# Performance work log

Measured on AMD Instinct MI355X. Metric: run time of the kernel, lower is better.

Reference implementation:

```python
import jax, jax.numpy as jnp
import numpy as np


def _l2norm(x, eps=1e-6):
    # Matches F.normalize(p=2, dim=-1, eps=eps): divide by max(||x||, eps)
    n = jnp.sqrt(jnp.sum(x * x, axis=-1, keepdims=True))
    return x / jnp.maximum(n, eps)


def setup_inputs() -> dict:
    key = jax.random.key(0)
    k0, k1, k2, k3, k4 = jax.random.split(key, 5)
    B, T, H, Dk, Dv = 2, 4096, 16, 128, 128
    q = _l2norm(jax.random.normal(k0, (B, T, H, Dk), dtype=jnp.float32))
    k = _l2norm(jax.random.normal(k1, (B, T, H, Dk), dtype=jnp.float32))
    v = jax.random.normal(k2, (B, T, H, Dv), dtype=jnp.float32)
    # alpha: decay in (0,1) (module: exp(-exp(A_log)*softplus(a+dt_bias)))
    alpha = jax.random.uniform(k3, (B, T, H), dtype=jnp.float32, minval=0.5, maxval=0.999)
    # beta: write gate in (0,1) (module: sigmoid(b))
    beta = jax.random.uniform(k4, (B, T, H), dtype=jnp.float32, minval=0.01, maxval=0.99)
    initial_state = jnp.zeros((B, H, Dk, Dv), dtype=jnp.float32)
    return {"q": q, "k": k, "v": v, "alpha": alpha, "beta": beta,
            "initial_state": initial_state}


def reference(q, k, v, alpha, beta, initial_state):
    """Gated delta rule recurrence (faithful to gdn_recurrent_naive).

    S_t = a_t * (S_{t-1} - b_t * k_t (k_t^T S_{t-1})) + b_t * k_t v_t^T
    o_t = S_t^T q_t
    """
    def step(S, xs):
        q_t, k_t, v_t, a_t, b_t = xs  # (B,H,Dk), (B,H,Dk), (B,H,Dv), (B,H), (B,H)
        a = a_t[..., None, None]
        b = b_t[..., None, None]
        kS = jnp.einsum('bhd,bhdv->bhv', k_t, S)          # k^T S
        S = a * (S - b * jnp.einsum('bhd,bhv->bhdv', k_t, kS)) \
            + b * jnp.einsum('bhd,bhv->bhdv', k_t, v_t)   # delta-rule update
        o = jnp.einsum('bhdv,bhd->bhv', S, q_t)           # read with q
        return S, o

    xs = (q.swapaxes(0, 1), k.swapaxes(0, 1), v.swapaxes(0, 1),
          alpha.swapaxes(0, 1), beta.swapaxes(0, 1))  # time-major for scan
    S_final, outs = jax.lax.scan(step, initial_state.astype(jnp.float32), xs)
    return outs.swapaxes(0, 1), S_final  # (B,T,H,Dv), (B,H,Dk,Dv)
```

## Files before the change

### kernel.cpp

```cpp
#include <hip/hip_runtime.h>

#define T_LEN 4096
#define H_N   16
#define DK    128
#define DV    128
#define LCH   64
#define NCH   64

typedef float f32x4 __attribute__((ext_vector_type(4)));
typedef short s16x8 __attribute__((ext_vector_type(8)));

#define OFF_U0 0
#define OFF_W  32768
#define OFF_Q  49152
#define OFF_KD 65536
#define OFF_G  81920
#define OFF_GM 90112
#define CH_B   90368ull
#define WS_NEED (2048ull * CH_B)

#define SWZ(row) (((row)&7) << 4)

#define AST 68
#define RST 132

__device__ __forceinline__ unsigned short f2b(float x) {
  unsigned u = __float_as_uint(x);
  return (unsigned short)((u + 0x7FFF + ((u >> 16) & 1)) >> 16);
}

#define GLDS16(gp, lp)                                                        \
  __builtin_amdgcn_global_load_lds(                                           \
      (const __attribute__((address_space(1))) void*)(gp),                    \
      (__attribute__((address_space(3))) void*)(lp), 16, 0, 0)
#define GLDS4(gp, lp)                                                         \
  __builtin_amdgcn_global_load_lds(                                           \
      (const __attribute__((address_space(1))) void*)(gp),                    \
      (__attribute__((address_space(3))) void*)(lp), 4, 0, 0)

#define LBAR()                                                                \
  do {                                                                        \
    asm volatile("s_waitcnt lgkmcnt(0)" ::: "memory");                        \
    __builtin_amdgcn_s_barrier();                                             \
    __builtin_amdgcn_sched_barrier(0);                                        \
  } while (0)

__device__ void solve64(float* RHS, const float* A, int tid) {
#pragma unroll 1
  for (int I = 0; I < 4; ++I) {
    if (I > 0) {
      const int i2 = 16 * I + (tid >> 4), cg = tid & 15;
      float* rp = RHS + i2 * RST + cg * 8;
      f32x4 a0 = *(const f32x4*)(rp);
      f32x4 a1 = *(const f32x4*)(rp + 4);
      for (int j = 0; j < 16 * I; ++j) {
        float a = A[i2 * AST + j];
        const float* yp = RHS + j * RST + cg * 8;
        f32x4 y0 = *(const f32x4*)(yp);
        f32x4 y1 = *(const f32x4*)(yp + 4);
#pragma unroll
        for (int e = 0; e < 4; ++e) {
          a0[e] = fmaf(-a, y0[e], a0[e]);
          a1[e] = fmaf(-a, y1[e], a1[e]);
        }
      }
      *(f32x4*)(rp) = a0;
      *(f32x4*)(rp + 4) = a1;
      __syncthreads();
    }
    if (tid < 128) {
      const int col = tid;
      float y[16];
#pragma unroll
      for (int r = 0; r < 16; ++r) y[r] = RHS[(16 * I + r) * RST + col];
#pragma unroll
      for (int r = 1; r < 16; ++r) {
        float t0 = 0.f, t1 = 0.f;
#pragma unroll
        for (int j = 0; j < 15; ++j)
          if (j < r) {
            float av = A[(16 * I + r) * AST + 16 * I + j];
            if (j & 1) t1 = fmaf(av, y[j], t1);
            else       t0 = fmaf(av, y[j], t0);
          }
        y[r] -= t0 + t1;
      }
#pragma unroll
      for (int r = 0; r < 16; ++r) RHS[(16 * I + r) * RST + col] = y[r];
    }
    __syncthreads();
  }
}

extern "C" __global__ void __launch_bounds__(256) gdn_p1(
    const float* __restrict__ q, const float* __restrict__ k,
    const float* __restrict__ v, const float* __restrict__ al,
    const float* __restrict__ be, char* __restrict__ ws) {
  __shared__ __align__(16) unsigned char big[34048];
  __shared__ __align__(16) float A_s[64 * AST];
  __shared__ float g_s[64], bb_s[64], sc_s[64];
  unsigned char* Kb = big;
  unsigned char* Qb = big + 16384;
  float* RHS = (float*)big;

  const int bid = blockIdx.x;
  const int bh = bid & 31, c = bid >> 5;
  const int b = bh >> 4, h = bh & 15;
  const int tid = threadIdx.x;
  const int t0 = c * LCH;
  char* wsc = ws + (size_t)(bh * 64 + c) * CH_B;

  if (tid < 64) {
    size_t gi = (size_t)(b * T_LEN + t0 + tid) * H_N + h;
    float x = __logf(al[gi]);
    bb_s[tid] = be[gi];
#pragma unroll
    for (int d = 1; d < 64; d <<= 1) {
      float yv = __shfl_up(x, d, 64);
      if (tid >= d) x += yv;
    }
    float gam = __expf(x);
    g_s[tid] = x;
    sc_s[tid] = gam;
    *(float*)(wsc + OFF_GM + tid * 4) = gam;
  }

  for (int idx = tid; idx < 1024; idx += 256) {
    int row = idx >> 4, grp = idx & 15;
    size_t go = ((size_t)(b * T_LEN + t0 + row) * H_N + h) * DK + grp * 8;
    float4 ka = *(const float4*)(k + go);
    float4 kb2 = *(const float4*)(k + go + 4);
    float4 qa = *(const float4*)(q + go);
    float4 qb2 = *(const float4*)(q + go + 4);
    union { unsigned short u[8]; uint4 v4; } tk, tq;
    tk.u[0] = f2b(ka.x); tk.u[1] = f2b(ka.y); tk.u[2] = f2b(ka.z); tk.u[3] = f2b(ka.w);
    tk.u[4] = f2b(kb2.x); tk.u[5] = f2b(kb2.y); tk.u[6] = f2b(kb2.z); tk.u[7] = f2b(kb2.w);
    tq.u[0] = f2b(qa.x); tq.u[1] = f2b(qa.y); tq.u[2] = f2b(qa.z); tq.u[3] = f2b(qa.w);
    tq.u[4] = f2b(qb2.x); tq.u[5] = f2b(qb2.y); tq.u[6] = f2b(qb2.z); tq.u[7] = f2b(qb2.w);
    int la = (row * 256 + grp * 16) ^ SWZ(row);
    *(uint4*)(Kb + la) = tk.v4;
    *(uint4*)(Qb + la) = tq.v4;
    *(uint4*)(wsc + OFF_Q + la) = tq.v4;
  }
  __syncthreads();

  const int w = tid >> 6, l = tid & 63, li = l & 15, hi = l >> 4;
  f32x4 aK[4], aQ[4];
#pragma unroll
  for (int jt = 0; jt < 4; ++jt) { aK[jt] = (f32x4){0, 0, 0, 0}; aQ[jt] = (f32x4){0, 0, 0, 0}; }
#pragma unroll
  for (int ks = 0; ks < 4; ++ks) {
    int rowA = 16 * w + li;
    int oa = (rowA * 256 + ks * 64 + hi * 16) ^ SWZ(rowA);
    s16x8 fa = *(const s16x8*)(Kb + oa);
    s16x8 fq = *(const s16x8*)(Qb + oa);
#pragma unroll
    for (int jt = 0; jt < 4; ++jt) {
      int rowB = 16 * jt + li;
      s16x8 fb = *(const s16x8*)(Kb + ((rowB * 256 + ks * 64 + hi * 16) ^ SWZ(rowB)));
      aK[jt] = __builtin_amdgcn_mfma_f32_16x16x32_bf16(fa, fb, aK[jt], 0, 0, 0);
      aQ[jt] = __builtin_amdgcn_mfma_f32_16x16x32_bf16(fq, fb, aQ[jt], 0, 0, 0);
    }
  }
#pragma unroll
  for (int jt = 0; jt < 4; ++jt)
#pragma unroll
    for (int r = 0; r < 4; ++r) {
      int i = 16 * w + hi * 4 + r, j = 16 * jt + li;
      float e = __expf(g_s[i] - g_s[j]);
      A_s[i * AST + j] = (j < i) ? bb_s[i] * e * aK[jt][r] : 0.f;
      *(unsigned short*)(wsc + OFF_G + ((i * 128 + j * 2) ^ SWZ(i))) =
          f2b((j <= i) ? e * aQ[jt][r] : 0.f);
    }
  __syncthreads();

  for (int idx = tid; idx < 2048; idx += 256) {
    int row = idx >> 5, c4 = idx & 31;
    float4 vv = *(const float4*)(v + ((size_t)(b * T_LEN + t0 + row) * H_N + h) * DV + c4 * 4);
    float s = bb_s[row];
    float4 o = {s * vv.x, s * vv.y, s * vv.z, s * vv.w};
    *(float4*)(RHS + row * RST + c4 * 4) = o;
  }
  __syncthreads();
  solve64(RHS, A_s, tid);
  for (int idx = tid; idx < 2048; idx += 256) {
    int row = idx >> 5, c4 = idx & 31;
    *(float4*)(wsc + OFF_U0 + (c4 >> 2) * 4096 + row * 64 + (c4 & 3) * 16) =
        *(const float4*)(RHS + row * RST + c4 * 4);
  }
  __syncthreads();

  for (int idx = tid; idx < 2048; idx += 256) {
    int row = idx >> 5, c4 = idx & 31;
    float4 kv = *(const float4*)(k + ((size_t)(b * T_LEN + t0 + row) * H_N + h) * DK + c4 * 4);
    float s = bb_s[row] * sc_s[row];
    float4 o = {s * kv.x, s * kv.y, s * kv.z, s * kv.w};
    *(float4*)(RHS + row * RST + c4 * 4) = o;
  }
  __syncthreads();
  solve64(RHS, A_s, tid);
  for (int idx = tid; idx < 1024; idx += 256) {
    int row = idx >> 4, g8 = idx & 15;
    const float* p = RHS + row * RST + g8 * 8;
    union { unsigned short u[8]; uint4 v4; } t;
#pragma unroll
    for (int e = 0; e < 8; ++e) t.u[e] = f2b(-p[e]);
    *(uint4*)(wsc + OFF_W + ((row * 256 + g8 * 16) ^ SWZ(row))) = t.v4;
  }
  __syncthreads();

  if (tid < 64) sc_s[tid] = __expf(g_s[63] - g_s[tid]);
  __syncthreads();
  float* Kf = (float*)big;
#pragma unroll 1
  for (int p = 0; p < 2; ++p) {
    for (int idx = tid; idx < 1024; idx += 256) {
      int r = idx >> 5, c4 = idx & 31;
      float4 kv = *(const float4*)(k + ((size_t)(b * T_LEN + t0 + 32 * p + r) * H_N + h) * DK + c4 * 4);
      *(float4*)(Kf + r * 132 + c4 * 4) = kv;
    }
    __syncthreads();
#pragma unroll
    for (int m = 0; m < 16; ++m) {
      int flat = m * 256 + tid;
      int j32 = flat & 31, d = flat >> 5;
      float val = sc_s[32 * p + j32] * Kf[j32 * 132 + d];
      *(unsigned short*)(wsc + OFF_KD + ((d * 128 + (32 * p + j32) * 2) ^ SWZ(d))) = f2b(val);
    }
    __syncthreads();
  }
}

extern "C" __global__ void __launch_bounds__(512, 1) gdn_p2(
    const float* __restrict__ S0, float* __restrict__ out,
    const char* __restrict__ ws) {
  __shared__ unsigned char Wb[2][16384];
  __shared__ unsigned char Qb[2][16384];
  __shared__ unsigned char KDb[2][16384];
  __shared__ unsigned char Gb[2][8192];
  __shared__ float U0s[2][1024];
  __shared__ float gam[2][64];
  __shared__ unsigned char Stb[4096];
  __shared__ unsigned char Ytb[2048];
  __shared__ float Oa[1024];

  const int bid = blockIdx.x;
  const int bh = bid & 31, s = bid >> 5;
  const int b = bh >> 4, h = bh & 15;
  const int tid = threadIdx.x;
  const int w = tid >> 6;
  const int lane = tid & 63, li = lane & 15, hi = lane >> 4;
  const int wq = w & 3;
  const bool grpA = (w < 4);
  const char* wsbase = ws + (size_t)bh * 64 * CH_B;

#define STG(CI, P)                                                            \
  do {                                                                        \
    const char* c_ = wsbase + (size_t)(CI) * CH_B;                            \
    _Pragma("unroll") for (int j_ = 0; j_ < 2; ++j_) {                        \
      GLDS16(c_ + OFF_W + j_ * 8192 + tid * 16, &Wb[P][j_ * 8192 + w * 1024]); \
      GLDS16(c_ + OFF_Q + j_ * 8192 + tid * 16, &Qb[P][j_ * 8192 + w * 1024]); \
      GLDS16(c_ + OFF_KD + j_ * 8192 + tid * 16, &KDb[P][j_ * 8192 + w * 1024]); \
    }                                                                         \
    GLDS16(c_ + OFF_G + tid * 16, &Gb[P][w * 1024]);                          \
    if (w < 4) GLDS16(c_ + OFF_U0 + s * 4096 + tid * 16,                      \
                      (unsigned char*)U0s[P] + w * 1024);                     \
    if (w == 7) GLDS4(c_ + OFF_GM + lane * 4, &gam[P][0]);                    \
  } while (0)

  float S[2][4];
  if (!grpA) {
#pragma unroll
    for (int t = 0; t < 2; ++t)
#pragma unroll
      for (int r = 0; r < 4; ++r) {
        int d = (wq + 4 * t) * 16 + hi * 4 + r;
        S[t][r] = S0[((size_t)bh * 128 + d) * 128 + s * 16 + li];
      }
  }
#define WRITE_ST()                                                            \
  do {                                                                        \
    _Pragma("unroll") for (int t = 0; t < 2; ++t)                             \
        _Pragma("unroll") for (int r = 0; r < 4; r += 2) {                    \
      int d = (wq + 4 * t) * 16 + hi * 4 + r;                                 \
      unsigned pk = (unsigned)f2b(S[t][r]) | ((unsigned)f2b(S[t][r + 1]) << 16); \
      *(unsigned*)(Stb + ((li * 256 + d * 2) ^ SWZ(li))) = pk;                \
    }                                                                         \
  } while (0)

  STG(0, 0);
  if (!grpA) WRITE_ST();
  __syncthreads();

#pragma unroll 1
  for (int c = 0; c < NCH; ++c) {
    const int p = c & 1;
    if (c + 1 < NCH) STG(c + 1, p ^ 1);

    s16x8 sfb[4];
#pragma unroll
    for (int ks = 0; ks < 4; ++ks)
      sfb[ks] = *(const s16x8*)(Stb + ((li * 256 + ks * 64 + hi * 16) ^ SWZ(li)));

    if (grpA) {
      f32x4 Y;
#pragma unroll
      for (int r = 0; r < 4; ++r) Y[r] = U0s[p][(16 * wq + hi * 4 + r) * 16 + li];
#pragma unroll
      for (int ks = 0; ks < 4; ++ks) {
        s16x8 fa = *(const s16x8*)(Wb[p] + (((16 * wq + li) * 256 + ks * 64 + hi * 16) ^ SWZ(li)));
        Y = __builtin_amdgcn_mfma_f32_16x16x32_bf16(fa, sfb[ks], Y, 0, 0, 0);
      }
#pragma unroll
      for (int r = 0; r < 4; r += 2) {
        int j = 16 * wq + hi * 4 + r;
        unsigned pk = (unsigned)f2b(Y[r]) | ((unsigned)f2b(Y[r + 1]) << 16);
        *(unsigned*)(Ytb + ((li * 128 + j * 2) ^ SWZ(li))) = pk;
      }
      LBAR();
      f32x4 O;
      s16x8 yfb[2];
#pragma unroll
      for (int ks = 0; ks < 2; ++ks)
        yfb[ks] = *(const s16x8*)(Ytb + ((li * 128 + ks * 64 + hi * 16) ^ SWZ(li)));
#pragma unroll
      for (int r = 0; r < 4; ++r) O[r] = Oa[(16 * wq + hi * 4 + r) * 16 + li];
#pragma unroll
      for (int ks = 0; ks < 2; ++ks) {
        s16x8 fa = *(const s16x8*)(Gb[p] + (((16 * wq + li) * 128 + ks * 64 + hi * 16) ^ SWZ(li)));
        O = __builtin_amdgcn_mfma_f32_16x16x32_bf16(fa, yfb[ks], O, 0, 0, 0);
      }
#pragma unroll
      for (int r = 0; r < 4; ++r) {
        size_t oi = ((size_t)(b * T_LEN + c * 64 + 16 * wq + hi * 4 + r) * H_N + h) * DV + s * 16 + li;
        out[oi] = O[r];
      }
    } else {
      f32x4 Oq = {0, 0, 0, 0};
#pragma unroll
      for (int ks = 0; ks < 4; ++ks) {
        s16x8 fa = *(const s16x8*)(Qb[p] + (((16 * wq + li) * 256 + ks * 64 + hi * 16) ^ SWZ(li)));
        Oq = __builtin_amdgcn_mfma_f32_16x16x32_bf16(fa, sfb[ks], Oq, 0, 0, 0);
      }
#pragma unroll
      for (int r = 0; r < 4; ++r) {
        int row = 16 * wq + hi * 4 + r;
        Oa[row * 16 + li] = gam[p][row] * Oq[r];
      }
      LBAR();
      s16x8 yfb[2];
#pragma unroll
      for (int ks = 0; ks < 2; ++ks)
        yfb[ks] = *(const s16x8*)(Ytb + ((li * 128 + ks * 64 + hi * 16) ^ SWZ(li)));
      float ge = gam[p][63];
#pragma unroll
      for (int t = 0; t < 2; ++t) {
        f32x4 acc;
#pragma unroll
        for (int r = 0; r < 4; ++r) acc[r] = ge * S[t][r];
#pragma unroll
        for (int ks = 0; ks < 2; ++ks) {
          s16x8 fa = *(const s16x8*)(KDb[p] + ((((wq + 4 * t) * 16 + li) * 128 + ks * 64 + hi * 16) ^ SWZ(li)));
          acc = __builtin_amdgcn_mfma_f32_16x16x32_bf16(fa, yfb[ks], acc, 0, 0, 0);
        }
#pragma unroll
        for (int r = 0; r < 4; ++r) S[t][r] = acc[r];
      }
      WRITE_ST();
    }
    __syncthreads();
  }

  if (!grpA) {
#pragma unroll
    for (int t = 0; t < 2; ++t)
#pragma unroll
      for (int r = 0; r < 4; ++r) {
        int d = (wq + 4 * t) * 16 + hi * 4 + r;
        out[(size_t)(2 * T_LEN * H_N * DV) + ((size_t)bh * 128 + d) * 128 + s * 16 + li] = S[t][r];
      }
  }
}

#define COLS 16
#define CHUNK 16
#define STEP_B 8192u
#define AB_B 64u
#define OSTRIDE (H_N * DV)
template <int CTRL>
__device__ __forceinline__ float dpp_add(float x) {
  int y = __builtin_amdgcn_update_dpp(0, __float_as_int(x), CTRL, 0xF, 0xF, true);
  return x + __int_as_float(y);
}
__device__ __forceinline__ float red16(float x) {
  x = dpp_add<0xB1>(x); x = dpp_add<0x4E>(x);
  x = dpp_add<0x124>(x); x = dpp_add<0x128>(x);
  return x;
}
extern "C" __global__ void __launch_bounds__(256, 1) gdn_fallback(
    const float* __restrict__ q, const float* __restrict__ k,
    const float* __restrict__ v, const float* __restrict__ al,
    const float* __restrict__ be, const float* __restrict__ S0,
    float* __restrict__ out) {
  __shared__ float kb[2][CHUNK * DK];
  __shared__ float qb[2][CHUNK * DK];
  __shared__ float vb[2][CHUNK * COLS];
  __shared__ float abuf[2][64];
  __shared__ float bbuf[2][64];
  const int bid = blockIdx.x;
  const int bh = bid & 31, g = bid >> 5;
  const int b = bh >> 4, h = bh & 15;
  const int tid = threadIdx.x;
  const int cl = tid >> 4, li = tid & 15, lane = tid & 63, wid = tid >> 6;
  const int col = g * COLS + cl, d0 = li * 8;
  const size_t bh_qk = ((size_t)b * T_LEN * H_N + h) * DK;
  const size_t bh_v = ((size_t)b * T_LEN * H_N + h) * DV;
  const size_t bh_ab = (size_t)b * T_LEN * H_N + h;
  const int fo0 = wid * 2048 + lane * 16, fo1 = fo0 + 1024;
  const char* kg0 = (const char*)(k + bh_qk) + (size_t)(fo0 >> 9) * STEP_B + (fo0 & 511);
  const char* kg1 = (const char*)(k + bh_qk) + (size_t)(fo1 >> 9) * STEP_B + (fo1 & 511);
  const char* qg0 = (const char*)(q + bh_qk) + (size_t)(fo0 >> 9) * STEP_B + (fo0 & 511);
  const char* qg1 = (const char*)(q + bh_qk) + (size_t)(fo1 >> 9) * STEP_B + (fo1 & 511);
  const int fv = lane * 16;
  const char* vg = (const char*)(v + bh_v + g * COLS) + (size_t)(fv >> 6) * STEP_B + (fv & 63);
  const int lcl = lane < 16 ? lane : 15;
  const char* ag = (const char*)(al + bh_ab) + (size_t)lcl * AB_B;
  const char* bg = (const char*)(be + bh_ab) + (size_t)lcl * AB_B;
#define STAGEF(CI, P) do { \
    const size_t off = (size_t)(CI) * (CHUNK * STEP_B); \
    const size_t offab = (size_t)(CI) * (CHUNK * AB_B); \
    GLDS16(kg0 + off, &kb[P][wid * 512]); GLDS16(kg1 + off, &kb[P][wid * 512 + 256]); \
    GLDS16(qg0 + off, &qb[P][wid * 512]); GLDS16(qg1 + off, &qb[P][wid * 512 + 256]); \
    if (wid == 0) GLDS16(vg + off, &vb[P][0]); \
    else if (wid == 1) GLDS4(ag + offab, &abuf[P][0]); \
    else if (wid == 2) GLDS4(bg + offab, &bbuf[P][0]); \
  } while (0)
  float sv[8];
  const float* s0p = S0 + ((size_t)(b * H_N + h) * DK + d0) * DV + col;
#pragma unroll
  for (int j = 0; j < 8; ++j) sv[j] = s0p[(size_t)j * DV];
  STAGEF(0, 0);
  __syncthreads();
  float* op = out + bh_v + col;
  for (int ci = 0; ci < T_LEN / CHUNK; ++ci) {
    const int p = ci & 1;
    if (ci + 1 < T_LEN / CHUNK) STAGEF(ci + 1, p ^ 1);
    const float* kc = kb[p]; const float* qc = qb[p]; const float* vc = vb[p];
    const float* ac = abuf[p]; const float* bc = bbuf[p];
#pragma unroll
    for (int j = 0; j < CHUNK; ++j) {
      f32x4 kA = *(const f32x4*)(kc + j * DK + d0);
      f32x4 kB = *(const f32x4*)(kc + j * DK + d0 + 4);
      f32x4 qA = *(const f32x4*)(qc + j * DK + d0);
      f32x4 qB = *(const f32x4*)(qc + j * DK + d0 + 4);
      float vv = vc[j * COLS + cl], aa = ac[j], bv = bc[j];
      float kk[8] = {kA[0], kA[1], kA[2], kA[3], kB[0], kB[1], kB[2], kB[3]};
      float qq[8] = {qA[0], qA[1], qA[2], qA[3], qB[0], qB[1], qB[2], qB[3]};
      float pk0 = kk[0] * sv[0], pk1 = kk[1] * sv[1];
      float pu0 = qq[0] * sv[0], pu1 = qq[1] * sv[1];
      float pg0 = kk[0] * qq[0], pg1 = kk[1] * qq[1];
#pragma unroll
      for (int m = 2; m < 8; m += 2) {
        pk0 = fmaf(kk[m], sv[m], pk0); pk1 = fmaf(kk[m + 1], sv[m + 1], pk1);
        pu0 = fmaf(qq[m], sv[m], pu0); pu1 = fmaf(qq[m + 1], sv[m + 1], pu1);
        pg0 = fmaf(kk[m], qq[m], pg0); pg1 = fmaf(kk[m + 1], qq[m + 1], pg1);
      }
      float pk = red16(pk0 + pk1), pu = red16(pu0 + pu1), pg = red16(pg0 + pg1);
      float tmp = fmaf(-(bv * aa), pk, bv * vv);
#pragma unroll
      for (int m = 0; m < 8; ++m) sv[m] = fmaf(aa, sv[m], kk[m] * tmp);
      if (li == 0) op[(size_t)(ci * CHUNK + j) * OSTRIDE] = fmaf(pg, tmp, aa * pu);
    }
    __syncthreads();
  }
  float* sf = out + (size_t)2 * T_LEN * H_N * DV + ((size_t)(b * H_N + h) * DK + d0) * DV + col;
#pragma unroll
  for (int j = 0; j < 8; ++j) sf[(size_t)j * DV] = sv[j];
}

extern "C" void kernel_launch(void* const* d_in, const int* in_sizes, int n_in,
                              void* d_out, int out_size, void* d_ws,
                              size_t ws_size, hipStream_t stream) {
  const float* q = (const float*)d_in[0];
  const float* k = (const float*)d_in[1];
  const float* v = (const float*)d_in[2];
  const float* al = (const float*)d_in[3];
  const float* be = (const float*)d_in[4];
  const float* S0 = (const float*)d_in[5];
  float* out = (float*)d_out;

  if (ws_size >= WS_NEED) {
    gdn_p1<<<dim3(2048), dim3(256), 0, stream>>>(q, k, v, al, be, (char*)d_ws);
    gdn_p2<<<dim3(256), dim3(512), 0, stream>>>(S0, out, (const char*)d_ws);
  } else {
    gdn_fallback<<<dim3(256), dim3(256), 0, stream>>>(q, k, v, al, be, S0, out);
  }
}
```

Baseline: 282.0 us.

## Load per-chunk MFMA operands directly from global into registers, drop LDS staging

Removes the double-buffered LDS staging of W, Q, KD, G, U0 and gamma in the gdn_p2 kernel. Each wave now reads its MFMA fragments straight from the workspace in global memory at the start of each chunk, and the __syncthreads calls become LBAR. This cuts LDS traffic and footprint and shortens the async-copy path. The cost is that global load latency now sits on the sequential chunk critical path with no prefetch of the next chunk, and the swizzled 16-byte reads go to global memory, where they may coalesce poorly.

```diff
diff --git a/kernel.cpp b/kernel.cpp
--- a/kernel.cpp
+++ b/kernel.cpp
@@ -234,12 +234,6 @@
 extern "C" __global__ void __launch_bounds__(512, 1) gdn_p2(
     const float* __restrict__ S0, float* __restrict__ out,
     const char* __restrict__ ws) {
-  __shared__ unsigned char Wb[2][16384];
-  __shared__ unsigned char Qb[2][16384];
-  __shared__ unsigned char KDb[2][16384];
-  __shared__ unsigned char Gb[2][8192];
-  __shared__ float U0s[2][1024];
-  __shared__ float gam[2][64];
   __shared__ unsigned char Stb[4096];
   __shared__ unsigned char Ytb[2048];
   __shared__ float Oa[1024];
@@ -254,20 +248,6 @@
   const bool grpA = (w < 4);
   const char* wsbase = ws + (size_t)bh * 64 * CH_B;
 
-#define STG(CI, P)                                                            \
-  do {                                                                        \
-    const char* c_ = wsbase + (size_t)(CI) * CH_B;                            \
-    _Pragma("unroll") for (int j_ = 0; j_ < 2; ++j_) {                        \
-      GLDS16(c_ + OFF_W + j_ * 8192 + tid * 16, &Wb[P][j_ * 8192 + w * 1024]); \
-      GLDS16(c_ + OFF_Q + j_ * 8192 + tid * 16, &Qb[P][j_ * 8192 + w * 1024]); \
-      GLDS16(c_ + OFF_KD + j_ * 8192 + tid * 16, &KDb[P][j_ * 8192 + w * 1024]); \
-    }                                                                         \
-    GLDS16(c_ + OFF_G + tid * 16, &Gb[P][w * 1024]);                          \
-    if (w < 4) GLDS16(c_ + OFF_U0 + s * 4096 + tid * 16,                      \
-                      (unsigned char*)U0s[P] + w * 1024);                     \
-    if (w == 7) GLDS4(c_ + OFF_GM + lane * 4, &gam[P][0]);                    \
-  } while (0)
-
   float S[2][4];
   if (!grpA) {
 #pragma unroll
@@ -288,14 +268,45 @@
     }                                                                         \
   } while (0)
 
-  STG(0, 0);
   if (!grpA) WRITE_ST();
-  __syncthreads();
+  LBAR();
 
 #pragma unroll 1
   for (int c = 0; c < NCH; ++c) {
-    const int p = c & 1;
-    if (c + 1 < NCH) STG(c + 1, p ^ 1);
+    const char* c_ = wsbase + (size_t)c * CH_B;
+
+    s16x8 fA[4], fB[2], fB2[2];
+    f32x4 u0;
+    float gr[4], ge = 0.f;
+    if (grpA) {
+#pragma unroll
+      for (int ks = 0; ks < 4; ++ks)
+        fA[ks] = *(const s16x8*)(c_ + OFF_W +
+                    (((16 * wq + li) * 256 + ks * 64 + hi * 16) ^ SWZ(li)));
+#pragma unroll
+      for (int ks = 0; ks < 2; ++ks)
+        fB[ks] = *(const s16x8*)(c_ + OFF_G +
+                    (((16 * wq + li) * 128 + ks * 64 + hi * 16) ^ SWZ(li)));
+#pragma unroll
+      for (int r = 0; r < 4; ++r)
+        u0[r] = *(const float*)(c_ + OFF_U0 + s * 4096 +
+                                ((16 * wq + hi * 4 + r) * 16 + li) * 4);
+    } else {
+#pragma unroll
+      for (int ks = 0; ks < 4; ++ks)
+        fA[ks] = *(const s16x8*)(c_ + OFF_Q +
+                    (((16 * wq + li) * 256 + ks * 64 + hi * 16) ^ SWZ(li)));
+#pragma unroll
+      for (int t = 0; t < 2; ++t)
+#pragma unroll
+        for (int ks = 0; ks < 2; ++ks)
+          ((t == 0) ? fB : fB2)[ks] = *(const s16x8*)(c_ + OFF_KD +
+              ((((wq + 4 * t) * 16 + li) * 128 + ks * 64 + hi * 16) ^ SWZ(li)));
+#pragma unroll
+      for (int r = 0; r < 4; ++r)
+        gr[r] = *(const float*)(c_ + OFF_GM + (16 * wq + hi * 4 + r) * 4);
+      ge = *(const float*)(c_ + OFF_GM + 63 * 4);
+    }
 
     s16x8 sfb[4];
 #pragma unroll
@@ -303,14 +314,10 @@
       sfb[ks] = *(const s16x8*)(Stb + ((li * 256 + ks * 64 + hi * 16) ^ SWZ(li)));
 
     if (grpA) {
-      f32x4 Y;
-#pragma unroll
-      for (int r = 0; r < 4; ++r) Y[r] = U0s[p][(16 * wq + hi * 4 + r) * 16 + li];
-#pragma unroll
-      for (int ks = 0; ks < 4; ++ks) {
-        s16x8 fa = *(const s16x8*)(Wb[p] + (((16 * wq + li) * 256 + ks * 64 + hi * 16) ^ SWZ(li)));
-        Y = __builtin_amdgcn_mfma_f32_16x16x32_bf16(fa, sfb[ks], Y, 0, 0, 0);
-      }
+      f32x4 Y = u0;
+#pragma unroll
+      for (int ks = 0; ks < 4; ++ks)
+        Y = __builtin_amdgcn_mfma_f32_16x16x32_bf16(fA[ks], sfb[ks], Y, 0, 0, 0);
 #pragma unroll
       for (int r = 0; r < 4; r += 2) {
         int j = 16 * wq + hi * 4 + r;
@@ -318,18 +325,16 @@
         *(unsigned*)(Ytb + ((li * 128 + j * 2) ^ SWZ(li))) = pk;
       }
       LBAR();
-      f32x4 O;
       s16x8 yfb[2];
 #pragma unroll
       for (int ks = 0; ks < 2; ++ks)
         yfb[ks] = *(const s16x8*)(Ytb + ((li * 128 + ks * 64 + hi * 16) ^ SWZ(li)));
+      f32x4 O;
 #pragma unroll
       for (int r = 0; r < 4; ++r) O[r] = Oa[(16 * wq + hi * 4 + r) * 16 + li];
 #pragma unroll
-      for (int ks = 0; ks < 2; ++ks) {
-        s16x8 fa = *(const s16x8*)(Gb[p] + (((16 * wq + li) * 128 + ks * 64 + hi * 16) ^ SWZ(li)));
-        O = __builtin_amdgcn_mfma_f32_16x16x32_bf16(fa, yfb[ks], O, 0, 0, 0);
-      }
+      for (int ks = 0; ks < 2; ++ks)
+        O = __builtin_amdgcn_mfma_f32_16x16x32_bf16(fB[ks], yfb[ks], O, 0, 0, 0);
 #pragma unroll
       for (int r = 0; r < 4; ++r) {
         size_t oi = ((size_t)(b * T_LEN + c * 64 + 16 * wq + hi * 4 + r) * H_N + h) * DV + s * 16 + li;
@@ -338,37 +343,41 @@
     } else {
       f32x4 Oq = {0, 0, 0, 0};
 #pragma unroll
-      for (int ks = 0; ks < 4; ++ks) {
-        s16x8 fa = *(const s16x8*)(Qb[p] + (((16 * wq + li) * 256 + ks * 64 + hi * 16) ^ SWZ(li)));
-        Oq = __builtin_amdgcn_mfma_f32_16x16x32_bf16(fa, sfb[ks], Oq, 0, 0, 0);
-      }
+      for (int ks = 0; ks < 4; ++ks)
+        Oq = __builtin_amdgcn_mfma_f32_16x16x32_bf16(fA[ks], sfb[ks], Oq, 0, 0, 0);
 #pragma unroll
       for (int r = 0; r < 4; ++r) {
         int row = 16 * wq + hi * 4 + r;
-        Oa[row * 16 + li] = gam[p][row] * Oq[r];
+        Oa[row * 16 + li] = gr[r] * Oq[r];
       }
       LBAR();
       s16x8 yfb[2];
 #pragma unroll
       for (int ks = 0; ks < 2; ++ks)
         yfb[ks] = *(const s16x8*)(Ytb + ((li * 128 + ks * 64 + hi * 16) ^ SWZ(li)));
-      float ge = gam[p][63];
-#pragma unroll
-      for (int t = 0; t < 2; ++t) {
+      {
         f32x4 acc;
 #pragma unroll
-        for (int r = 0; r < 4; ++r) acc[r] = ge * S[t][r];
-#pragma unroll
-        for (int ks = 0; ks < 2; ++ks) {
-          s16x8 fa = *(const s16x8*)(KDb[p] + ((((wq + 4 * t) * 16 + li) * 128 + ks * 64 + hi * 16) ^ SWZ(li)));
-          acc = __builtin_amdgcn_mfma_f32_16x16x32_bf16(fa, yfb[ks], acc, 0, 0, 0);
-        }
-#pragma unroll
-        for (int r = 0; r < 4; ++r) S[t][r] = acc[r];
+        for (int r = 0; r < 4; ++r) acc[r] = ge * S[0][r];
+#pragma unroll
+        for (int ks = 0; ks < 2; ++ks)
+          acc = __builtin_amdgcn_mfma_f32_16x16x32_bf16(fB[ks], yfb[ks], acc, 0, 0, 0);
+#pragma unroll
+        for (int r = 0; r < 4; ++r) S[0][r] = acc[r];
+      }
+      {
+        f32x4 acc;
+#pragma unroll
+        for (int r = 0; r < 4; ++r) acc[r] = ge * S[1][r];
+#pragma unroll
+        for (int ks = 0; ks < 2; ++ks)
+          acc = __builtin_amdgcn_mfma_f32_16x16x32_bf16(fB2[ks], yfb[ks], acc, 0, 0, 0);
+#pragma unroll
+        for (int r = 0; r < 4; ++r) S[1][r] = acc[r];
       }
       WRITE_ST();
     }
-    __syncthreads();
+    LBAR();
   }
 
   if (!grpA) {
```

Measured after the change: 263.9 us. 1.07x faster.

## Prefetch chunk operands directly into registers and rework triangular solve partitioning

Applied to the files above, without the earlier changes.

The recurrence kernel stops staging W, Q, KD, G, U0 and gamma through double-buffered LDS with global_load_lds. Each wave now loads its own MFMA fragments straight from global memory into register sets that alternate between chunks, with the loop unrolled by two. This removes the LDS staging traffic and most of the shared memory footprint, at the cost of higher register pressure and more uncoalesced 16-byte global loads sitting on the serial chunk path. Separately, the blocked forward-substitution update in solve64 now runs on 128 threads, each handling four rows by four columns, which reuses each RHS load across four rows but leaves half the block idle.

```diff
diff --git a/kernel.cpp b/kernel.cpp
--- a/kernel.cpp
+++ b/kernel.cpp
@@ -49,23 +49,33 @@
 #pragma unroll 1
   for (int I = 0; I < 4; ++I) {
     if (I > 0) {
-      const int i2 = 16 * I + (tid >> 4), cg = tid & 15;
-      float* rp = RHS + i2 * RST + cg * 8;
-      f32x4 a0 = *(const f32x4*)(rp);
-      f32x4 a1 = *(const f32x4*)(rp + 4);
-      for (int j = 0; j < 16 * I; ++j) {
-        float a = A[i2 * AST + j];
-        const float* yp = RHS + j * RST + cg * 8;
-        f32x4 y0 = *(const f32x4*)(yp);
-        f32x4 y1 = *(const f32x4*)(yp + 4);
-#pragma unroll
-        for (int e = 0; e < 4; ++e) {
-          a0[e] = fmaf(-a, y0[e], a0[e]);
-          a1[e] = fmaf(-a, y1[e], a1[e]);
+      if (tid < 128) {
+        const int rg = tid >> 5;
+        const int r0 = 16 * I + rg * 4;
+        const int cs = (tid & 31) * 4;
+        f32x4 acc0 = *(const f32x4*)(RHS + (r0 + 0) * RST + cs);
+        f32x4 acc1 = *(const f32x4*)(RHS + (r0 + 1) * RST + cs);
+        f32x4 acc2 = *(const f32x4*)(RHS + (r0 + 2) * RST + cs);
+        f32x4 acc3 = *(const f32x4*)(RHS + (r0 + 3) * RST + cs);
+        for (int j = 0; j < 16 * I; ++j) {
+          f32x4 yv = *(const f32x4*)(RHS + j * RST + cs);
+          float a0 = A[(r0 + 0) * AST + j];
+          float a1 = A[(r0 + 1) * AST + j];
+          float a2 = A[(r0 + 2) * AST + j];
+          float a3 = A[(r0 + 3) * AST + j];
+#pragma unroll
+          for (int e = 0; e < 4; ++e) {
+            acc0[e] = fmaf(-a0, yv[e], acc0[e]);
+            acc1[e] = fmaf(-a1, yv[e], acc1[e]);
+            acc2[e] = fmaf(-a2, yv[e], acc2[e]);
+            acc3[e] = fmaf(-a3, yv[e], acc3[e]);
+          }
         }
+        *(f32x4*)(RHS + (r0 + 0) * RST + cs) = acc0;
+        *(f32x4*)(RHS + (r0 + 1) * RST + cs) = acc1;
+        *(f32x4*)(RHS + (r0 + 2) * RST + cs) = acc2;
+        *(f32x4*)(RHS + (r0 + 3) * RST + cs) = acc3;
       }
-      *(f32x4*)(rp) = a0;
-      *(f32x4*)(rp + 4) = a1;
       __syncthreads();
     }
     if (tid < 128) {
@@ -231,15 +241,106 @@
   }
 }
 
+#define DECLBUF(S)                                                            \
+  s16x8 fA0##S, fA1##S, fA2##S, fA3##S, fB0##S, fB1##S, fC0##S, fC1##S;       \
+  f32x4 u0##S;                                                                \
+  float gr0##S, gr1##S, gr2##S, gr3##S, ge##S;
+
+#define LOADC(S, CI)                                                          \
+  do {                                                                        \
+    const char* c_ = wsbase + (size_t)(CI) * CH_B;                            \
+    if (grpA) {                                                               \
+      fA0##S = *(const s16x8*)(c_ + OFF_W + (((16 * wq + li) * 256 + 0 * 64 + hi * 16) ^ SWZ(li))); \
+      fA1##S = *(const s16x8*)(c_ + OFF_W + (((16 * wq + li) * 256 + 1 * 64 + hi * 16) ^ SWZ(li))); \
+      fA2##S = *(const s16x8*)(c_ + OFF_W + (((16 * wq + li) * 256 + 2 * 64 + hi * 16) ^ SWZ(li))); \
+      fA3##S = *(const s16x8*)(c_ + OFF_W + (((16 * wq + li) * 256 + 3 * 64 + hi * 16) ^ SWZ(li))); \
+      fB0##S = *(const s16x8*)(c_ + OFF_G + (((16 * wq + li) * 128 + 0 * 64 + hi * 16) ^ SWZ(li))); \
+      fB1##S = *(const s16x8*)(c_ + OFF_G + (((16 * wq + li) * 128 + 1 * 64 + hi * 16) ^ SWZ(li))); \
+      _Pragma("unroll") for (int r_ = 0; r_ < 4; ++r_)                        \
+        u0##S[r_] = *(const float*)(c_ + OFF_U0 + s * 4096 +                  \
+                                    ((16 * wq + hi * 4 + r_) * 16 + li) * 4); \
+    } else {                                                                  \
+      fA0##S = *(const s16x8*)(c_ + OFF_Q + (((16 * wq + li) * 256 + 0 * 64 + hi * 16) ^ SWZ(li))); \
+      fA1##S = *(const s16x8*)(c_ + OFF_Q + (((16 * wq + li) * 256 + 1 * 64 + hi * 16) ^ SWZ(li))); \
+      fA2##S = *(const s16x8*)(c_ + OFF_Q + (((16 * wq + li) * 256 + 2 * 64 + hi * 16) ^ SWZ(li))); \
+      fA3##S = *(const s16x8*)(c_ + OFF_Q + (((16 * wq + li) * 256 + 3 * 64 + hi * 16) ^ SWZ(li))); \
+      fB0##S = *(const s16x8*)(c_ + OFF_KD + ((((wq + 0) * 16 + li) * 128 + 0 * 64 + hi * 16) ^ SWZ(li))); \
+      fB1##S = *(const s16x8*)(c_ + OFF_KD + ((((wq + 0) * 16 + li) * 128 + 1 * 64 + hi * 16) ^ SWZ(li))); \
+      fC0##S = *(const s16x8*)(c_ + OFF_KD + ((((wq + 4) * 16 + li) * 128 + 0 * 64 + hi * 16) ^ SWZ(li))); \
+      fC1##S = *(const s16x8*)(c_ + OFF_KD + ((((wq + 4) * 16 + li) * 128 + 1 * 64 + hi * 16) ^ SWZ(li))); \
+      gr0##S = *(const float*)(c_ + OFF_GM + (16 * wq + hi * 4 + 0) * 4);     \
+      gr1##S = *(const float*)(c_ + OFF_GM + (16 * wq + hi * 4 + 1) * 4);     \
+      gr2##S = *(const float*)(c_ + OFF_GM + (16 * wq + hi * 4 + 2) * 4);     \
+      gr3##S = *(const float*)(c_ + OFF_GM + (16 * wq + hi * 4 + 3) * 4);     \
+      ge##S = *(const float*)(c_ + OFF_GM + 63 * 4);                          \
+    }                                                                         \
+  } while (0)
+
+#define BODY(CUR, NXT, c)                                                     \
+  do {                                                                        \
+    if ((c) + 1 < NCH) LOADC(NXT, (c) + 1);                                   \
+    s16x8 sfb0 = *(const s16x8*)(Stb + ((li * 256 + 0 * 64 + hi * 16) ^ SWZ(li))); \
+    s16x8 sfb1 = *(const s16x8*)(Stb + ((li * 256 + 1 * 64 + hi * 16) ^ SWZ(li))); \
+    s16x8 sfb2 = *(const s16x8*)(Stb + ((li * 256 + 2 * 64 + hi * 16) ^ SWZ(li))); \
+    s16x8 sfb3 = *(const s16x8*)(Stb + ((li * 256 + 3 * 64 + hi * 16) ^ SWZ(li))); \
+    if (grpA) {                                                               \
+      f32x4 Y = u0##CUR;                                                      \
+      Y = __builtin_amdgcn_mfma_f32_16x16x32_bf16(fA0##CUR, sfb0, Y, 0, 0, 0); \
+      Y = __builtin_amdgcn_mfma_f32_16x16x32_bf16(fA1##CUR, sfb1, Y, 0, 0, 0); \
+      Y = __builtin_amdgcn_mfma_f32_16x16x32_bf16(fA2##CUR, sfb2, Y, 0, 0, 0); \
+      Y = __builtin_amdgcn_mfma_f32_16x16x32_bf16(fA3##CUR, sfb3, Y, 0, 0, 0); \
+      _Pragma("unroll") for (int r_ = 0; r_ < 4; r_ += 2) {                   \
+        int j_ = 16 * wq + hi * 4 + r_;                                       \
+        unsigned pk_ = (unsigned)f2b(Y[r_]) | ((unsigned)f2b(Y[r_ + 1]) << 16); \
+        *(unsigned*)(Ytb + ((li * 128 + j_ * 2) ^ SWZ(li))) = pk_;            \
+      }                                                                       \
+      LBAR();                                                                 \
+      s16x8 yfb0 = *(const s16x8*)(Ytb + ((li * 128 + 0 * 64 + hi * 16) ^ SWZ(li))); \
+      s16x8 yfb1 = *(const s16x8*)(Ytb + ((li * 128 + 1 * 64 + hi * 16) ^ SWZ(li))); \
+      f32x4 O;                                                                \
+      _Pragma("unroll") for (int r_ = 0; r_ < 4; ++r_)                        \
+        O[r_] = Oa[(16 * wq + hi * 4 + r_) * 16 + li];                        \
+      O = __builtin_amdgcn_mfma_f32_16x16x32_bf16(fB0##CUR, yfb0, O, 0, 0, 0); \
+      O = __builtin_amdgcn_mfma_f32_16x16x32_bf16(fB1##CUR, yfb1, O, 0, 0, 0); \
+      _Pragma("unroll") for (int r_ = 0; r_ < 4; ++r_) {                      \
+        size_t oi_ = ((size_t)(b * T_LEN + (c) * 64 + 16 * wq + hi * 4 + r_) * H_N + h) * DV + s * 16 + li; \
+        out[oi_] = O[r_];                                                     \
+      }                                                                       \
+    } else {                                                                  \
+      f32x4 Oq = {0, 0, 0, 0};                                                \
+      Oq = __builtin_amdgcn_mfma_f32_16x16x32_bf16(fA0##CUR, sfb0, Oq, 0, 0, 0); \
+      Oq = __builtin_amdgcn_mfma_f32_16x16x32_bf16(fA1##CUR, sfb1, Oq, 0, 0, 0); \
+      Oq = __builtin_amdgcn_mfma_f32_16x16x32_bf16(fA2##CUR, sfb2, Oq, 0, 0, 0); \
+      Oq = __builtin_amdgcn_mfma_f32_16x16x32_bf16(fA3##CUR, sfb3, Oq, 0, 0, 0); \
+      Oa[(16 * wq + hi * 4 + 0) * 16 + li] = gr0##CUR * Oq[0];                \
+      Oa[(16 * wq + hi * 4 + 1) * 16 + li] = gr1##CUR * Oq[1];                \
+      Oa[(16 * wq + hi * 4 + 2) * 16 + li] = gr2##CUR * Oq[2];                \
+      Oa[(16 * wq + hi * 4 + 3) * 16 + li] = gr3##CUR * Oq[3];                \
+      LBAR();                                                                 \
+      s16x8 yfb0 = *(const s16x8*)(Ytb + ((li * 128 + 0 * 64 + hi * 16) ^ SWZ(li))); \
+      s16x8 yfb1 = *(const s16x8*)(Ytb + ((li * 128 + 1 * 64 + hi * 16) ^ SWZ(li))); \
+      {                                                                       \
+        f32x4 acc;                                                            \
+        _Pragma("unroll") for (int r_ = 0; r_ < 4; ++r_) acc[r_] = ge##CUR * S[0][r_]; \
+        acc = __builtin_amdgcn_mfma_f32_16x16x32_bf16(fB0##CUR, yfb0, acc, 0, 0, 0); \
+        acc = __builtin_amdgcn_mfma_f32_16x16x32_bf16(fB1##CUR, yfb1, acc, 0, 0, 0); \
+        _Pragma("unroll") for (int r_ = 0; r_ < 4; ++r_) S[0][r_] = acc[r_];  \
+      }                                                                       \
+      {                                                                       \
+        f32x4 acc;                                                            \
+        _Pragma("unroll") for (int r_ = 0; r_ < 4; ++r_) acc[r_] = ge##CUR * S[1][r_]; \
+        acc = __builtin_amdgcn_mfma_f32_16x16x32_bf16(fC0##CUR, yfb0, acc, 0, 0, 0); \
+        acc = __builtin_amdgcn_mfma_f32_16x16x32_bf16(fC1##CUR, yfb1, acc, 0, 0, 0); \
+        _Pragma("unroll") for (int r_ = 0; r_ < 4; ++r_) S[1][r_] = acc[r_];  \
+      }                                                                       \
+      WRITE_ST();                                                             \
+    }                                                                         \
+    LBAR();                                                                   \
+  } while (0)
+
 extern "C" __global__ void __launch_bounds__(512, 1) gdn_p2(
     const float* __restrict__ S0, float* __restrict__ out,
     const char* __restrict__ ws) {
-  __shared__ unsigned char Wb[2][16384];
-  __shared__ unsigned char Qb[2][16384];
-  __shared__ unsigned char KDb[2][16384];
-  __shared__ unsigned char Gb[2][8192];
-  __shared__ float U0s[2][1024];
-  __shared__ float gam[2][64];
   __shared__ unsigned char Stb[4096];
   __shared__ unsigned char Ytb[2048];
   __shared__ float Oa[1024];
@@ -254,20 +355,6 @@
   const bool grpA = (w < 4);
   const char* wsbase = ws + (size_t)bh * 64 * CH_B;
 
-#define STG(CI, P)                                                            \
-  do {                                                                        \
-    const char* c_ = wsbase + (size_t)(CI) * CH_B;                            \
-    _Pragma("unroll") for (int j_ = 0; j_ < 2; ++j_) {                        \
-      GLDS16(c_ + OFF_W + j_ * 8192 + tid * 16, &Wb[P][j_ * 8192 + w * 1024]); \
-      GLDS16(c_ + OFF_Q + j_ * 8192 + tid * 16, &Qb[P][j_ * 8192 + w * 1024]); \
-      GLDS16(c_ + OFF_KD + j_ * 8192 + tid * 16, &KDb[P][j_ * 8192 + w * 1024]); \
-    }                                                                         \
-    GLDS16(c_ + OFF_G + tid * 16, &Gb[P][w * 1024]);                          \
-    if (w < 4) GLDS16(c_ + OFF_U0 + s * 4096 + tid * 16,                      \
-                      (unsigned char*)U0s[P] + w * 1024);                     \
-    if (w == 7) GLDS4(c_ + OFF_GM + lane * 4, &gam[P][0]);                    \
-  } while (0)
-
   float S[2][4];
   if (!grpA) {
 #pragma unroll
@@ -288,87 +375,16 @@
     }                                                                         \
   } while (0)
 
-  STG(0, 0);
   if (!grpA) WRITE_ST();
-  __syncthreads();
+  DECLBUF(A_)
+  DECLBUF(B_)
+  LOADC(A_, 0);
+  LBAR();
 
 #pragma unroll 1
-  for (int c = 0; c < NCH; ++c) {
-    const int p = c & 1;
-    if (c + 1 < NCH) STG(c + 1, p ^ 1);
-
-    s16x8 sfb[4];
-#pragma unroll
-    for (int ks = 0; ks < 4; ++ks)
-      sfb[ks] = *(const s16x8*)(Stb + ((li * 256 + ks * 64 + hi * 16) ^ SWZ(li)));
-
-    if (grpA) {
-      f32x4 Y;
-#pragma unroll
-      for (int r = 0; r < 4; ++r) Y[r] = U0s[p][(16 * wq + hi * 4 + r) * 16 + li];
-#pragma unroll
-      for (int ks = 0; ks < 4; ++ks) {
-        s16x8 fa = *(const s16x8*)(Wb[p] + (((16 * wq + li) * 256 + ks * 64 + hi * 16) ^ SWZ(li)));
-        Y = __builtin_amdgcn_mfma_f32_16x16x32_bf16(fa, sfb[ks], Y, 0, 0, 0);
-      }
-#pragma unroll
-      for (int r = 0; r < 4; r += 2) {
-        int j = 16 * wq + hi * 4 + r;
-        unsigned pk = (unsigned)f2b(Y[r]) | ((unsigned)f2b(Y[r + 1]) << 16);
-        *(unsigned*)(Ytb + ((li * 128 + j * 2) ^ SWZ(li))) = pk;
-      }
-      LBAR();
-      f32x4 O;
-      s16x8 yfb[2];
-#pragma unroll
-      for (int ks = 0; ks < 2; ++ks)
-        yfb[ks] = *(const s16x8*)(Ytb + ((li * 128 + ks * 64 + hi * 16) ^ SWZ(li)));
-#pragma unroll
-      for (int r = 0; r < 4; ++r) O[r] = Oa[(16 * wq + hi * 4 + r) * 16 + li];
-#pragma unroll
-      for (int ks = 0; ks < 2; ++ks) {
-        s16x8 fa = *(const s16x8*)(Gb[p] + (((16 * wq + li) * 128 + ks * 64 + hi * 16) ^ SWZ(li)));
-        O = __builtin_amdgcn_mfma_f32_16x16x32_bf16(fa, yfb[ks], O, 0, 0, 0);
-      }
-#pragma unroll
-      for (int r = 0; r < 4; ++r) {
-        size_t oi = ((size_t)(b * T_LEN + c * 64 + 16 * wq + hi * 4 + r) * H_N + h) * DV + s * 16 + li;
-        out[oi] = O[r];
-      }
-    } else {
-      f32x4 Oq = {0, 0, 0, 0};
-#pragma unroll
-      for (int ks = 0; ks < 4; ++ks) {
-        s16x8 fa = *(const s16x8*)(Qb[p] + (((16 * wq + li) * 256 + ks * 64 + hi * 16) ^ SWZ(li)));
-        Oq = __builtin_amdgcn_mfma_f32_16x16x32_bf16(fa, sfb[ks], Oq, 0, 0, 0);
-      }
-#pragma unroll
-      for (int r = 0; r < 4; ++r) {
-        int row = 16 * wq + hi * 4 + r;
-        Oa[row * 16 + li] = gam[p][row] * Oq[r];
-      }
-      LBAR();
-      s16x8 yfb[2];
-#pragma unroll
-      for (int ks = 0; ks < 2; ++ks)
-        yfb[ks] = *(const s16x8*)(Ytb + ((li * 128 + ks * 64 + hi * 16) ^ SWZ(li)));
-      float ge = gam[p][63];
-#pragma unroll
-      for (int t = 0; t < 2; ++t) {
-        f32x4 acc;
-#pragma unroll
-        for (int r = 0; r < 4; ++r) acc[r] = ge * S[t][r];
-#pragma unroll
-        for (int ks = 0; ks < 2; ++ks) {
-          s16x8 fa = *(const s16x8*)(KDb[p] + ((((wq + 4 * t) * 16 + li) * 128 + ks * 64 + hi * 16) ^ SWZ(li)));
-          acc = __builtin_amdgcn_mfma_f32_16x16x32_bf16(fa, yfb[ks], acc, 0, 0, 0);
-        }
-#pragma unroll
-        for (int r = 0; r < 4; ++r) S[t][r] = acc[r];
-      }
-      WRITE_ST();
-    }
-    __syncthreads();
+  for (int cc = 0; cc < NCH; cc += 2) {
+    BODY(A_, B_, cc);
+    BODY(B_, A_, cc + 1);
   }
 
   if (!grpA) {
```

New measurement: 256.4 us. -9.1%, faster.
